# Optimization experiments

Hardware: AMD Instinct MI355X
Metric: run time of the kernel (lower is better)

The kernel has to match this reference:

```python
import jax, jax.numpy as jnp
import numpy as np
from jax import lax

D_MODEL = 512
NUM_HEADS = 8
HEAD_DIM = D_MODEL // NUM_HEADS
KERNEL = 3
B, S = 8, 1024


def _conv1d(x, w, b):
    # x: [B, Cin, S], w: [Cout, Cin, K], 'same' padding, dilation 1
    y = lax.conv_general_dilated(x, w, window_strides=(1,), padding='SAME',
                                 dimension_numbers=('NCH', 'OIH', 'NCH'))
    return y + b[None, :, None]


def setup_inputs() -> dict:
    key = jax.random.key(0)
    ks = jax.random.split(key, 12)
    # conv weight init: normal(0, sqrt(2/(k*out_channels))) with out_channels=head_dim per head;
    # stacking H per-head convs gives a single [D, D, K] weight (head-major out channels).
    std_qk = np.sqrt(2.0 / (KERNEL * HEAD_DIM))
    std_v = np.sqrt(2.0 / (1 * HEAD_DIM))
    inp = {
        'query': jax.random.normal(ks[0], (B, S, D_MODEL), jnp.float32),
        'key_t': jax.random.normal(ks[1], (B, S, D_MODEL), jnp.float32),
        'value': jax.random.normal(ks[2], (B, S, D_MODEL), jnp.float32),
        'Wq': jax.random.normal(ks[3], (D_MODEL, D_MODEL, KERNEL), jnp.float32) * std_qk,
        'bq': jnp.full((D_MODEL,), 0.1, jnp.float32),
        'Wk': jax.random.normal(ks[4], (D_MODEL, D_MODEL, KERNEL), jnp.float32) * std_qk,
        'bk': jnp.full((D_MODEL,), 0.1, jnp.float32),
        'Wv': jax.random.normal(ks[5], (D_MODEL, D_MODEL, 1), jnp.float32) * std_v,
        'bv': jnp.full((D_MODEL,), 0.1, jnp.float32),
        'Wo': jax.random.normal(ks[6], (D_MODEL, D_MODEL), jnp.float32) * (1.0 / np.sqrt(D_MODEL)),
        'bo': jnp.zeros((D_MODEL,), jnp.float32),
    }
    return inp


def reference(query, key_t, value, Wq, bq, Wk, bk, Wv, bv, Wo, bo):
    Bb, Ss, D = query.shape
    H, hd = NUM_HEADS, HEAD_DIM
    # [B, D, S]
    q_ = jnp.transpose(query, (0, 2, 1))
    k_ = jnp.transpose(key_t, (0, 2, 1))
    v_ = jnp.transpose(value, (0, 2, 1))
    # per-head TCN projections fused into one conv; out channels head-major
    Q = _conv1d(q_, Wq, bq).reshape(Bb, H, hd, Ss)
    K = _conv1d(k_, Wk, bk).reshape(Bb, H, hd, Ss)
    V = _conv1d(v_, Wv, bv).reshape(Bb, H, hd, Ss)
    # scores scaled by head_dim (NOT sqrt), as in source
    scores = jnp.einsum('bhds,bhdt->bhst', Q, K) / hd
    attn = jax.nn.softmax(scores, axis=-1)          # [B,H,S,S]
    ave_att = attn.mean(axis=1)                      # [B,S,S]
    out = jnp.einsum('bhst,bhdt->bhsd', attn, V)     # [B,H,S,hd]
    out = jnp.transpose(out, (0, 2, 1, 3)).reshape(Bb, Ss, D)
    out = out @ Wo.T + bo                            # torch Linear: x W^T + b
    return out, ave_att
```

## Files before the change

kernel.cpp:

```cpp
#include <hip/hip_runtime.h>
#include <hip/hip_bf16.h>
#include <math.h>

#define BB 8
#define SS 1024
#define DM 512
#define NH 8
#define HD 64

typedef __attribute__((ext_vector_type(8))) short bf16x8;
typedef __attribute__((ext_vector_type(4))) float f32x4;
typedef __hip_bfloat16 bf16;

static __device__ __forceinline__ short f2bs(float f){
  return __builtin_bit_cast(short, __float2bfloat16(f));
}

static __device__ __forceinline__ float wave_max64(float v){
#pragma unroll
  for (int off = 32; off > 0; off >>= 1) v = fmaxf(v, __shfl_xor(v, off, 64));
  return v;
}
static __device__ __forceinline__ float wave_sum64(float v){
#pragma unroll
  for (int off = 32; off > 0; off >>= 1) v += __shfl_xor(v, off, 64);
  return v;
}

__global__ __launch_bounds__(256) void pack_w(
    const float* __restrict__ Wq, const float* __restrict__ Wk,
    const float* __restrict__ Wv, const float* __restrict__ Wo,
    bf16* __restrict__ Wqb, bf16* __restrict__ Wkb,
    bf16* __restrict__ Wvb, bf16* __restrict__ Wob)
{
  const int idx = blockIdx.x * 256 + threadIdx.x;
#pragma unroll
  for (int k = 0; k < 3; k++){
    Wqb[k * 262144 + idx] = __float2bfloat16(Wq[idx * 3 + k]);
    Wkb[k * 262144 + idx] = __float2bfloat16(Wk[idx * 3 + k]);
  }
  Wvb[idx] = __float2bfloat16(Wv[idx]);
  Wob[idx] = __float2bfloat16(Wo[idx]);
}

template<int KS, bool IN_BF16, bool OUT_F32, bool TROUT>
__global__ __launch_bounds__(256) void gemm_k(const void* __restrict__ xin,
    const bf16* __restrict__ Wb, const float* __restrict__ bias, void* __restrict__ outv)
{
  constexpr int ST = 32;
  constexpr int PAD = (KS - 1) / 2;
  constexpr int NR = ST + KS - 1;
  constexpr int LDX = DM + 8;
  constexpr int SMB_A = NR * LDX * 2;
  constexpr int SMB_B = 32 * 257 * 4;
  constexpr int SMB = (SMB_A > SMB_B) ? SMB_A : SMB_B;
  __shared__ char smem[SMB];
  bf16*  xs = (bf16*)smem;
  float* es = (float*)smem;

  const int b   = blockIdx.x / (SS / ST);
  const int s0  = (blockIdx.x % (SS / ST)) * ST;
  const int tid = threadIdx.x;
  const int w = tid >> 6, l = tid & 63;
  const int lr = l & 15, lg = l >> 4;
  const int o0 = w * 128;

  if (IN_BF16){
    const bf16* x = (const bf16*)xin;
    for (int idx = tid * 4; idx < NR * DM; idx += 1024){
      int r = idx >> 9, c = idx & 511;
      int srow = s0 - PAD + r;
      ushort4 v; v.x = v.y = v.z = v.w = 0;
      if (srow >= 0 && srow < SS)
        v = *reinterpret_cast<const ushort4*>(&x[((size_t)b * SS + srow) * DM + c]);
      *reinterpret_cast<ushort4*>(&xs[r * LDX + c]) = v;
    }
  } else {
    const float* x = (const float*)xin;
    for (int idx = tid * 4; idx < NR * DM; idx += 1024){
      int r = idx >> 9, c = idx & 511;
      int srow = s0 - PAD + r;
      float4 v = make_float4(0.f, 0.f, 0.f, 0.f);
      if (srow >= 0 && srow < SS)
        v = *reinterpret_cast<const float4*>(&x[((size_t)b * SS + srow) * DM + c]);
      ushort4 u;
      u.x = (unsigned short)f2bs(v.x); u.y = (unsigned short)f2bs(v.y);
      u.z = (unsigned short)f2bs(v.z); u.w = (unsigned short)f2bs(v.w);
      *reinterpret_cast<ushort4*>(&xs[r * LDX + c]) = u;
    }
  }

  float bs[8];
#pragma unroll
  for (int of = 0; of < 8; of++) bs[of] = bias[o0 + of * 16 + lr];

  __syncthreads();

  f32x4 acc[2][8];
#pragma unroll
  for (int sf = 0; sf < 2; sf++)
#pragma unroll
    for (int of = 0; of < 8; of++) acc[sf][of] = (f32x4){0.f, 0.f, 0.f, 0.f};

#pragma unroll
  for (int k = 0; k < KS; k++){
    const bf16* wbk = Wb + (size_t)k * DM * DM + (size_t)o0 * DM;
    for (int ic = 0; ic < 16; ic++){
      const int i0 = ic * 32 + lg * 8;
      bf16x8 a0 = *reinterpret_cast<const bf16x8*>(&xs[(lr +      k) * LDX + i0]);
      bf16x8 a1 = *reinterpret_cast<const bf16x8*>(&xs[(lr + 16 + k) * LDX + i0]);
#pragma unroll
      for (int of = 0; of < 8; of++){
        bf16x8 bw = *reinterpret_cast<const bf16x8*>(&wbk[(size_t)(of * 16 + lr) * DM + i0]);
        acc[0][of] = __builtin_amdgcn_mfma_f32_16x16x32_bf16(a0, bw, acc[0][of], 0, 0, 0);
        acc[1][of] = __builtin_amdgcn_mfma_f32_16x16x32_bf16(a1, bw, acc[1][of], 0, 0, 0);
      }
    }
  }

  for (int h2 = 0; h2 < 2; h2++){
    __syncthreads();
    if ((w >> 1) == h2){
      const int ob = (w & 1) * 128;
#pragma unroll
      for (int sf = 0; sf < 2; sf++)
#pragma unroll
        for (int of = 0; of < 8; of++)
#pragma unroll
          for (int r = 0; r < 4; r++)
            es[(sf * 16 + lg * 4 + r) * 257 + ob + of * 16 + lr] = acc[sf][of][r] + bs[of];
    }
    __syncthreads();
    if (!TROUT){
      for (int it = 0; it < 8; it++){
        int t = tid + it * 256;
        int s = t >> 6, c4 = (t & 63) * 4;
        const float* ep = &es[s * 257 + c4];
        if (OUT_F32){
          float* out = (float*)outv;
          float4 v = make_float4(ep[0], ep[1], ep[2], ep[3]);
          *reinterpret_cast<float4*>(&out[((size_t)b * SS + s0 + s) * DM + h2 * 256 + c4]) = v;
        } else {
          bf16* out = (bf16*)outv;
          ushort4 u;
          u.x = (unsigned short)f2bs(ep[0]); u.y = (unsigned short)f2bs(ep[1]);
          u.z = (unsigned short)f2bs(ep[2]); u.w = (unsigned short)f2bs(ep[3]);
          *reinterpret_cast<ushort4*>(&out[((size_t)b * SS + s0 + s) * DM + h2 * 256 + c4]) = u;
        }
      }
    } else {
      bf16* out = (bf16*)outv;
      for (int pass = 0; pass < 8; pass++){
        int oc = pass * 32 + (tid >> 3);
        int s4 = (tid & 7) * 4;
        ushort4 u;
        u.x = (unsigned short)f2bs(es[(s4 + 0) * 257 + oc]);
        u.y = (unsigned short)f2bs(es[(s4 + 1) * 257 + oc]);
        u.z = (unsigned short)f2bs(es[(s4 + 2) * 257 + oc]);
        u.w = (unsigned short)f2bs(es[(s4 + 3) * 257 + oc]);
        int o = h2 * 256 + oc;
        *reinterpret_cast<ushort4*>(&out[((size_t)b * DM + o) * SS + s0 + s4]) = u;
      }
    }
  }
}

#define LDS_SC 1028
__global__ __launch_bounds__(256) void attn2(const bf16* __restrict__ Q,
    const bf16* __restrict__ K, const bf16* __restrict__ Vt,
    bf16* __restrict__ Tw, float* __restrict__ ave)
{
  extern __shared__ float smem[];
  float* scoresL = smem;
  float* aveL    = smem + 16 * LDS_SC;

  const int b   = blockIdx.x >> 6;
  const int s0  = (blockIdx.x & 63) * 16;
  const int tid = threadIdx.x;
  const int w = tid >> 6, l = tid & 63;
  const int lr = l & 15, lg = l >> 4;

  for (int idx = tid; idx < 16 * LDS_SC; idx += 256) aveL[idx] = 0.f;

  const size_t xbase = (size_t)b * SS * DM;
  const size_t vbase = (size_t)b * DM * SS;

  for (int h = 0; h < NH; h++){
    const int hoff = h * HD;
    bf16x8 qa[2];
#pragma unroll
    for (int kk = 0; kk < 2; kk++)
      qa[kk] = *reinterpret_cast<const bf16x8*>(
          &Q[xbase + (size_t)(s0 + lr) * DM + hoff + kk * 32 + lg * 8]);

    for (int tf = 0; tf < 16; tf++){
      const int t0 = w * 256 + tf * 16;
      f32x4 c = (f32x4){0.f, 0.f, 0.f, 0.f};
#pragma unroll
      for (int kk = 0; kk < 2; kk++){
        bf16x8 kb = *reinterpret_cast<const bf16x8*>(
            &K[xbase + (size_t)(t0 + lr) * DM + hoff + kk * 32 + lg * 8]);
        c = __builtin_amdgcn_mfma_f32_16x16x32_bf16(qa[kk], kb, c, 0, 0, 0);
      }
#pragma unroll
      for (int r = 0; r < 4; r++)
        scoresL[(lg * 4 + r) * LDS_SC + t0 + lr] = c[r] * (1.f / 64.f);
    }
    __syncthreads();

    for (int rr = 0; rr < 4; rr++){
      const int q = w * 4 + rr;
      float sv[16];
      float m = -1e30f;
#pragma unroll
      for (int j = 0; j < 16; j++){
        sv[j] = scoresL[q * LDS_SC + l + 64 * j];
        m = fmaxf(m, sv[j]);
      }
      m = wave_max64(m);
      float sum = 0.f;
#pragma unroll
      for (int j = 0; j < 16; j++){ sv[j] = __expf(sv[j] - m); sum += sv[j]; }
      sum = wave_sum64(sum);
      const float inv = 1.f / sum;
#pragma unroll
      for (int j = 0; j < 16; j++){
        const float p = sv[j] * inv;
        scoresL[q * LDS_SC + l + 64 * j] = p;
        aveL[q * LDS_SC + l + 64 * j] += p;
      }
    }
    __syncthreads();

    f32x4 pacc[4];
#pragma unroll
    for (int df = 0; df < 4; df++) pacc[df] = (f32x4){0.f, 0.f, 0.f, 0.f};
    for (int ks8 = 0; ks8 < 8; ks8++){
      const int t0 = w * 256 + ks8 * 32;
      const float* pr = &scoresL[(size_t)lr * LDS_SC + t0 + lg * 8];
      float4 p0 = *reinterpret_cast<const float4*>(pr);
      float4 p1 = *reinterpret_cast<const float4*>(pr + 4);
      bf16x8 pa;
      pa[0] = f2bs(p0.x); pa[1] = f2bs(p0.y); pa[2] = f2bs(p0.z); pa[3] = f2bs(p0.w);
      pa[4] = f2bs(p1.x); pa[5] = f2bs(p1.y); pa[6] = f2bs(p1.z); pa[7] = f2bs(p1.w);
#pragma unroll
      for (int df = 0; df < 4; df++){
        bf16x8 vb = *reinterpret_cast<const bf16x8*>(
            &Vt[vbase + (size_t)(hoff + df * 16 + lr) * SS + t0 + lg * 8]);
        pacc[df] = __builtin_amdgcn_mfma_f32_16x16x32_bf16(pa, vb, pacc[df], 0, 0, 0);
      }
    }
    __syncthreads();

#pragma unroll
    for (int df = 0; df < 4; df++)
#pragma unroll
      for (int r = 0; r < 4; r++)
        scoresL[w * 1040 + (lg * 4 + r) * 65 + df * 16 + lr] = pacc[df][r];
    __syncthreads();
    for (int idx = tid; idx < 1024; idx += 256){
      const int q = idx >> 6, d = idx & 63;
      float s = scoresL[q * 65 + d] + scoresL[1040 + q * 65 + d]
              + scoresL[2080 + q * 65 + d] + scoresL[3120 + q * 65 + d];
      Tw[xbase + (size_t)(s0 + q) * DM + hoff + d] = __float2bfloat16(s);
    }
    __syncthreads();
  }

  for (int idx = tid; idx < 16 * SS; idx += 256){
    const int q = idx >> 10, t = idx & 1023;
    ave[((size_t)b * SS + s0 + q) * SS + t] = aveL[q * LDS_SC + t] * 0.125f;
  }
}

extern "C" void kernel_launch(void* const* d_in, const int* in_sizes, int n_in,
                              void* d_out, int out_size, void* d_ws, size_t ws_size,
                              hipStream_t stream)
{
  const float* query = (const float*)d_in[0];
  const float* key_t = (const float*)d_in[1];
  const float* value = (const float*)d_in[2];
  const float* Wq = (const float*)d_in[3];
  const float* bq = (const float*)d_in[4];
  const float* Wk = (const float*)d_in[5];
  const float* bk = (const float*)d_in[6];
  const float* Wv = (const float*)d_in[7];
  const float* bv = (const float*)d_in[8];
  const float* Wo = (const float*)d_in[9];
  const float* bo = (const float*)d_in[10];

  float* out = (float*)d_out;
  float* ave = out + (size_t)BB * SS * DM;

  char* wsb = (char*)d_ws;
  bf16* Qw  = (bf16*)(wsb);
  bf16* Kw  = (bf16*)(wsb + 8388608);
  bf16* Vt  = (bf16*)(wsb + 16777216);
  bf16* Tw  = (bf16*)(wsb + 25165824);
  bf16* Wqb = (bf16*)(wsb + 33554432);
  bf16* Wkb = (bf16*)(wsb + 35127296);
  bf16* Wvb = (bf16*)(wsb + 36700160);
  bf16* Wob = (bf16*)(wsb + 37224448);

  hipLaunchKernelGGL(pack_w, dim3(1024), dim3(256), 0, stream,
                     Wq, Wk, Wv, Wo, Wqb, Wkb, Wvb, Wob);

  const int g = BB * (SS / 32);
  hipLaunchKernelGGL((gemm_k<3, false, false, false>), dim3(g), dim3(256), 0, stream,
                     (const void*)query, Wqb, bq, (void*)Qw);
  hipLaunchKernelGGL((gemm_k<3, false, false, false>), dim3(g), dim3(256), 0, stream,
                     (const void*)key_t, Wkb, bk, (void*)Kw);
  hipLaunchKernelGGL((gemm_k<1, false, false, true>), dim3(g), dim3(256), 0, stream,
                     (const void*)value, Wvb, bv, (void*)Vt);

  const size_t asmem = (size_t)2 * 16 * LDS_SC * sizeof(float);
  hipFuncSetAttribute((const void*)attn2,
                      hipFuncAttributeMaxDynamicSharedMemorySize, (int)asmem);
  hipLaunchKernelGGL(attn2, dim3(BB * 64), dim3(256), asmem, stream,
                     Qw, Kw, Vt, Tw, ave);

  hipLaunchKernelGGL((gemm_k<1, true, true, false>), dim3(g), dim3(256), 0, stream,
                     (const void*)Tw, Wob, bo, (void*)out);
}
```

Before: 664.5 us.

## Parallelize attention across heads with bf16 prob buffer and separate head-mean reduction

Attention now launches one block per (batch, head, 16-query tile) instead of looping over all heads inside a block. Scores stay in registers for the softmax, and the bf16 probabilities are staged in swizzled LDS and also written to a global buffer. A separate reduce kernel sums that buffer over heads to form the averaged attention map. The projection GEMMs are re-tiled to 16-row tiles, split output halves across blocks, and use an XOR-swizzled LDS layout. This gives far more parallelism, but it adds heavy global traffic for the probability buffer and rounds the averaged map through bf16 probabilities.

```diff
diff --git a/kernel.cpp b/kernel.cpp
--- a/kernel.cpp
+++ b/kernel.cpp
@@ -1,6 +1,5 @@
 #include <hip/hip_runtime.h>
 #include <hip/hip_bf16.h>
-#include <math.h>
 
 #define BB 8
 #define SS 1024
@@ -12,19 +11,8 @@
 typedef __attribute__((ext_vector_type(4))) float f32x4;
 typedef __hip_bfloat16 bf16;
 
-static __device__ __forceinline__ short f2bs(float f){
-  return __builtin_bit_cast(short, __float2bfloat16(f));
-}
-
-static __device__ __forceinline__ float wave_max64(float v){
-#pragma unroll
-  for (int off = 32; off > 0; off >>= 1) v = fmaxf(v, __shfl_xor(v, off, 64));
-  return v;
-}
-static __device__ __forceinline__ float wave_sum64(float v){
-#pragma unroll
-  for (int off = 32; off > 0; off >>= 1) v += __shfl_xor(v, off, 64);
-  return v;
+static __device__ __forceinline__ unsigned short f2bs(float f){
+  return (unsigned short)__builtin_bit_cast(short, __float2bfloat16(f));
 }
 
 __global__ __launch_bounds__(256) void pack_w(
@@ -44,233 +32,247 @@
 }
 
 template<int KS, bool IN_BF16, bool OUT_F32, bool TROUT>
-__global__ __launch_bounds__(256) void gemm_k(const void* __restrict__ xin,
+__global__ __launch_bounds__(256) void gemm2(const void* __restrict__ xin,
     const bf16* __restrict__ Wb, const float* __restrict__ bias, void* __restrict__ outv)
 {
-  constexpr int ST = 32;
+  constexpr int ST = 16;
   constexpr int PAD = (KS - 1) / 2;
   constexpr int NR = ST + KS - 1;
-  constexpr int LDX = DM + 8;
-  constexpr int SMB_A = NR * LDX * 2;
-  constexpr int SMB_B = 32 * 257 * 4;
+  constexpr int SMB_A = NR * 1024;
+  constexpr int SMB_B = 16 * 260 * 4;
   constexpr int SMB = (SMB_A > SMB_B) ? SMB_A : SMB_B;
   __shared__ char smem[SMB];
-  bf16*  xs = (bf16*)smem;
+  char*  xs = smem;
   float* es = (float*)smem;
 
-  const int b   = blockIdx.x / (SS / ST);
-  const int s0  = (blockIdx.x % (SS / ST)) * ST;
+  const int oh = blockIdx.x & 1;
+  const int st = (blockIdx.x >> 1) & 63;
+  const int b  = blockIdx.x >> 7;
+  const int s0 = st * ST;
   const int tid = threadIdx.x;
   const int w = tid >> 6, l = tid & 63;
   const int lr = l & 15, lg = l >> 4;
-  const int o0 = w * 128;
-
-  if (IN_BF16){
-    const bf16* x = (const bf16*)xin;
-    for (int idx = tid * 4; idx < NR * DM; idx += 1024){
-      int r = idx >> 9, c = idx & 511;
-      int srow = s0 - PAD + r;
-      ushort4 v; v.x = v.y = v.z = v.w = 0;
-      if (srow >= 0 && srow < SS)
-        v = *reinterpret_cast<const ushort4*>(&x[((size_t)b * SS + srow) * DM + c]);
-      *reinterpret_cast<ushort4*>(&xs[r * LDX + c]) = v;
+  const int o0 = oh * 256 + w * 64;
+
+  for (int idx = tid * 4; idx < NR * DM; idx += 1024){
+    const int r = idx >> 9, c = idx & 511;
+    const int srow = s0 - PAD + r;
+    const int byte = r * 1024 + ((c * 2) ^ ((r & 7) << 4));
+    if (IN_BF16){
+      ushort4 v = {0, 0, 0, 0};
+      if (0 <= srow && srow < SS)
+        v = *reinterpret_cast<const ushort4*>((const bf16*)xin + ((size_t)b * SS + srow) * DM + c);
+      *reinterpret_cast<ushort4*>(xs + byte) = v;
+    } else {
+      float4 v = make_float4(0.f, 0.f, 0.f, 0.f);
+      if (0 <= srow && srow < SS)
+        v = *reinterpret_cast<const float4*>((const float*)xin + ((size_t)b * SS + srow) * DM + c);
+      ushort4 u; u.x = f2bs(v.x); u.y = f2bs(v.y); u.z = f2bs(v.z); u.w = f2bs(v.w);
+      *reinterpret_cast<ushort4*>(xs + byte) = u;
+    }
+  }
+
+  float bs[4];
+#pragma unroll
+  for (int of = 0; of < 4; of++) bs[of] = bias[o0 + of * 16 + lr];
+
+  __syncthreads();
+
+  f32x4 acc[4];
+#pragma unroll
+  for (int of = 0; of < 4; of++) acc[of] = (f32x4){0.f, 0.f, 0.f, 0.f};
+
+#pragma unroll
+  for (int k = 0; k < KS; k++){
+    const bf16* wbk = Wb + (size_t)k * DM * DM;
+    const int row = lr + k;
+    const int rswz = (row & 7) << 4;
+    for (int ic = 0; ic < 16; ic++){
+      bf16x8 a = *reinterpret_cast<const bf16x8*>(
+          xs + row * 1024 + (((ic * 32 + lg * 8) * 2) ^ rswz));
+#pragma unroll
+      for (int of = 0; of < 4; of++){
+        bf16x8 bw = *reinterpret_cast<const bf16x8*>(
+            wbk + (size_t)(o0 + of * 16 + lr) * DM + ic * 32 + lg * 8);
+        acc[of] = __builtin_amdgcn_mfma_f32_16x16x32_bf16(a, bw, acc[of], 0, 0, 0);
+      }
+    }
+  }
+
+  __syncthreads();
+#pragma unroll
+  for (int of = 0; of < 4; of++)
+#pragma unroll
+    for (int r = 0; r < 4; r++)
+      es[(lg * 4 + r) * 260 + w * 64 + of * 16 + lr] = acc[of][r] + bs[of];
+  __syncthreads();
+
+  if (!TROUT){
+#pragma unroll
+    for (int it = 0; it < 4; it++){
+      const int t = tid + it * 256;
+      const int s = t >> 6, c4 = (t & 63) * 4;
+      const float* ep = &es[s * 260 + c4];
+      if (OUT_F32){
+        float4 v = make_float4(ep[0], ep[1], ep[2], ep[3]);
+        *reinterpret_cast<float4*>((float*)outv + ((size_t)b * SS + s0 + s) * DM + oh * 256 + c4) = v;
+      } else {
+        ushort4 u; u.x = f2bs(ep[0]); u.y = f2bs(ep[1]); u.z = f2bs(ep[2]); u.w = f2bs(ep[3]);
+        *reinterpret_cast<ushort4*>((bf16*)outv + ((size_t)b * SS + s0 + s) * DM + oh * 256 + c4) = u;
+      }
     }
   } else {
-    const float* x = (const float*)xin;
-    for (int idx = tid * 4; idx < NR * DM; idx += 1024){
-      int r = idx >> 9, c = idx & 511;
-      int srow = s0 - PAD + r;
-      float4 v = make_float4(0.f, 0.f, 0.f, 0.f);
-      if (srow >= 0 && srow < SS)
-        v = *reinterpret_cast<const float4*>(&x[((size_t)b * SS + srow) * DM + c]);
-      ushort4 u;
-      u.x = (unsigned short)f2bs(v.x); u.y = (unsigned short)f2bs(v.y);
-      u.z = (unsigned short)f2bs(v.z); u.w = (unsigned short)f2bs(v.w);
-      *reinterpret_cast<ushort4*>(&xs[r * LDX + c]) = u;
-    }
-  }
-
-  float bs[8];
-#pragma unroll
-  for (int of = 0; of < 8; of++) bs[of] = bias[o0 + of * 16 + lr];
-
-  __syncthreads();
-
-  f32x4 acc[2][8];
-#pragma unroll
-  for (int sf = 0; sf < 2; sf++)
-#pragma unroll
-    for (int of = 0; of < 8; of++) acc[sf][of] = (f32x4){0.f, 0.f, 0.f, 0.f};
-
-#pragma unroll
-  for (int k = 0; k < KS; k++){
-    const bf16* wbk = Wb + (size_t)k * DM * DM + (size_t)o0 * DM;
-    for (int ic = 0; ic < 16; ic++){
-      const int i0 = ic * 32 + lg * 8;
-      bf16x8 a0 = *reinterpret_cast<const bf16x8*>(&xs[(lr +      k) * LDX + i0]);
-      bf16x8 a1 = *reinterpret_cast<const bf16x8*>(&xs[(lr + 16 + k) * LDX + i0]);
-#pragma unroll
-      for (int of = 0; of < 8; of++){
-        bf16x8 bw = *reinterpret_cast<const bf16x8*>(&wbk[(size_t)(of * 16 + lr) * DM + i0]);
-        acc[0][of] = __builtin_amdgcn_mfma_f32_16x16x32_bf16(a0, bw, acc[0][of], 0, 0, 0);
-        acc[1][of] = __builtin_amdgcn_mfma_f32_16x16x32_bf16(a1, bw, acc[1][of], 0, 0, 0);
-      }
-    }
-  }
-
-  for (int h2 = 0; h2 < 2; h2++){
-    __syncthreads();
-    if ((w >> 1) == h2){
-      const int ob = (w & 1) * 128;
-#pragma unroll
-      for (int sf = 0; sf < 2; sf++)
-#pragma unroll
-        for (int of = 0; of < 8; of++)
-#pragma unroll
-          for (int r = 0; r < 4; r++)
-            es[(sf * 16 + lg * 4 + r) * 257 + ob + of * 16 + lr] = acc[sf][of][r] + bs[of];
-    }
-    __syncthreads();
-    if (!TROUT){
-      for (int it = 0; it < 8; it++){
-        int t = tid + it * 256;
-        int s = t >> 6, c4 = (t & 63) * 4;
-        const float* ep = &es[s * 257 + c4];
-        if (OUT_F32){
-          float* out = (float*)outv;
-          float4 v = make_float4(ep[0], ep[1], ep[2], ep[3]);
-          *reinterpret_cast<float4*>(&out[((size_t)b * SS + s0 + s) * DM + h2 * 256 + c4]) = v;
-        } else {
-          bf16* out = (bf16*)outv;
-          ushort4 u;
-          u.x = (unsigned short)f2bs(ep[0]); u.y = (unsigned short)f2bs(ep[1]);
-          u.z = (unsigned short)f2bs(ep[2]); u.w = (unsigned short)f2bs(ep[3]);
-          *reinterpret_cast<ushort4*>(&out[((size_t)b * SS + s0 + s) * DM + h2 * 256 + c4]) = u;
-        }
-      }
-    } else {
-      bf16* out = (bf16*)outv;
-      for (int pass = 0; pass < 8; pass++){
-        int oc = pass * 32 + (tid >> 3);
-        int s4 = (tid & 7) * 4;
-        ushort4 u;
-        u.x = (unsigned short)f2bs(es[(s4 + 0) * 257 + oc]);
-        u.y = (unsigned short)f2bs(es[(s4 + 1) * 257 + oc]);
-        u.z = (unsigned short)f2bs(es[(s4 + 2) * 257 + oc]);
-        u.w = (unsigned short)f2bs(es[(s4 + 3) * 257 + oc]);
-        int o = h2 * 256 + oc;
-        *reinterpret_cast<ushort4*>(&out[((size_t)b * DM + o) * SS + s0 + s4]) = u;
-      }
-    }
-  }
-}
-
-#define LDS_SC 1028
-__global__ __launch_bounds__(256) void attn2(const bf16* __restrict__ Q,
+    const int o = oh * 256 + tid;
+    uint us[8];
+#pragma unroll
+    for (int j = 0; j < 8; j++){
+      const float lo = es[(2 * j) * 260 + tid];
+      const float hi = es[(2 * j + 1) * 260 + tid];
+      us[j] = (uint)f2bs(lo) | ((uint)f2bs(hi) << 16);
+    }
+    uint4* dst = reinterpret_cast<uint4*>((bf16*)outv + ((size_t)b * DM + o) * SS + s0);
+    dst[0] = make_uint4(us[0], us[1], us[2], us[3]);
+    dst[1] = make_uint4(us[4], us[5], us[6], us[7]);
+  }
+}
+
+template<int HG>
+__global__ __launch_bounds__(256) void attn3(const bf16* __restrict__ Q,
     const bf16* __restrict__ K, const bf16* __restrict__ Vt,
-    bf16* __restrict__ Tw, float* __restrict__ ave)
-{
-  extern __shared__ float smem[];
-  float* scoresL = smem;
-  float* aveL    = smem + 16 * LDS_SC;
-
-  const int b   = blockIdx.x >> 6;
-  const int s0  = (blockIdx.x & 63) * 16;
-  const int tid = threadIdx.x;
+    bf16* __restrict__ Tw, bf16* __restrict__ Pbuf, int h0)
+{
+  __shared__ char smem[33280];
+  char*  plds = smem;
+  float* red  = (float*)smem;
+  float* mxL  = (float*)(smem + 32768);
+  float* smL  = (float*)(smem + 33024);
+
+  const int qt   = blockIdx.x & 63;
+  const int rest = blockIdx.x >> 6;
+  const int hl   = rest & (HG - 1);
+  const int b    = rest / HG;
+  const int h    = h0 + hl;
+  const int s0   = qt * 16;
+  const int tid  = threadIdx.x;
   const int w = tid >> 6, l = tid & 63;
   const int lr = l & 15, lg = l >> 4;
-
-  for (int idx = tid; idx < 16 * LDS_SC; idx += 256) aveL[idx] = 0.f;
-
-  const size_t xbase = (size_t)b * SS * DM;
+  const int hoff = h * HD;
+  const size_t xb = (size_t)b * SS * DM;
+
+  bf16x8 qb0 = *reinterpret_cast<const bf16x8*>(&Q[xb + (size_t)(s0 + lr) * DM + hoff + lg * 8]);
+  bf16x8 qb1 = *reinterpret_cast<const bf16x8*>(&Q[xb + (size_t)(s0 + lr) * DM + hoff + 32 + lg * 8]);
+
+  f32x4 sc[16];
+#pragma unroll
+  for (int tf = 0; tf < 16; tf++){
+    const int t0 = w * 256 + tf * 16;
+    bf16x8 ka0 = *reinterpret_cast<const bf16x8*>(&K[xb + (size_t)(t0 + lr) * DM + hoff + lg * 8]);
+    bf16x8 ka1 = *reinterpret_cast<const bf16x8*>(&K[xb + (size_t)(t0 + lr) * DM + hoff + 32 + lg * 8]);
+    f32x4 c = (f32x4){0.f, 0.f, 0.f, 0.f};
+    c = __builtin_amdgcn_mfma_f32_16x16x32_bf16(ka0, qb0, c, 0, 0, 0);
+    c = __builtin_amdgcn_mfma_f32_16x16x32_bf16(ka1, qb1, c, 0, 0, 0);
+#pragma unroll
+    for (int r = 0; r < 4; r++) sc[tf][r] = c[r] * (1.f / 64.f);
+  }
+
+  float m = -1e30f;
+#pragma unroll
+  for (int tf = 0; tf < 16; tf++)
+#pragma unroll
+    for (int r = 0; r < 4; r++) m = fmaxf(m, sc[tf][r]);
+  m = fmaxf(m, __shfl_xor(m, 16, 64));
+  m = fmaxf(m, __shfl_xor(m, 32, 64));
+  if (l < 16) mxL[w * 16 + l] = m;
+  __syncthreads();
+  m = fmaxf(fmaxf(mxL[lr], mxL[16 + lr]), fmaxf(mxL[32 + lr], mxL[48 + lr]));
+
+  float sum = 0.f;
+#pragma unroll
+  for (int tf = 0; tf < 16; tf++)
+#pragma unroll
+    for (int r = 0; r < 4; r++){ sc[tf][r] = __expf(sc[tf][r] - m); sum += sc[tf][r]; }
+  sum += __shfl_xor(sum, 16, 64);
+  sum += __shfl_xor(sum, 32, 64);
+  if (l < 16) smL[w * 16 + l] = sum;
+  __syncthreads();
+  const float inv = 1.f / (smL[lr] + smL[16 + lr] + smL[32 + lr] + smL[48 + lr]);
+
+  const size_t pb = (((size_t)b * HG + hl) * SS + (s0 + lr)) * SS;
+  const int swz = (lr & 7) << 4;
+#pragma unroll
+  for (int tf = 0; tf < 16; tf++){
+    const int t = w * 256 + tf * 16 + lg * 4;
+    const uint u0 = (uint)f2bs(sc[tf][0] * inv) | ((uint)f2bs(sc[tf][1] * inv) << 16);
+    const uint u1 = (uint)f2bs(sc[tf][2] * inv) | ((uint)f2bs(sc[tf][3] * inv) << 16);
+    *reinterpret_cast<uint2*>(plds + lr * 2048 + ((2 * t) ^ swz)) = make_uint2(u0, u1);
+    *reinterpret_cast<uint2*>((char*)Pbuf + 2 * (pb + t)) = make_uint2(u0, u1);
+  }
+
   const size_t vbase = (size_t)b * DM * SS;
-
-  for (int h = 0; h < NH; h++){
-    const int hoff = h * HD;
-    bf16x8 qa[2];
-#pragma unroll
-    for (int kk = 0; kk < 2; kk++)
-      qa[kk] = *reinterpret_cast<const bf16x8*>(
-          &Q[xbase + (size_t)(s0 + lr) * DM + hoff + kk * 32 + lg * 8]);
-
-    for (int tf = 0; tf < 16; tf++){
-      const int t0 = w * 256 + tf * 16;
-      f32x4 c = (f32x4){0.f, 0.f, 0.f, 0.f};
-#pragma unroll
-      for (int kk = 0; kk < 2; kk++){
-        bf16x8 kb = *reinterpret_cast<const bf16x8*>(
-            &K[xbase + (size_t)(t0 + lr) * DM + hoff + kk * 32 + lg * 8]);
-        c = __builtin_amdgcn_mfma_f32_16x16x32_bf16(qa[kk], kb, c, 0, 0, 0);
-      }
-#pragma unroll
-      for (int r = 0; r < 4; r++)
-        scoresL[(lg * 4 + r) * LDS_SC + t0 + lr] = c[r] * (1.f / 64.f);
-    }
-    __syncthreads();
-
-    for (int rr = 0; rr < 4; rr++){
-      const int q = w * 4 + rr;
-      float sv[16];
-      float m = -1e30f;
-#pragma unroll
-      for (int j = 0; j < 16; j++){
-        sv[j] = scoresL[q * LDS_SC + l + 64 * j];
-        m = fmaxf(m, sv[j]);
-      }
-      m = wave_max64(m);
-      float sum = 0.f;
-#pragma unroll
-      for (int j = 0; j < 16; j++){ sv[j] = __expf(sv[j] - m); sum += sv[j]; }
-      sum = wave_sum64(sum);
-      const float inv = 1.f / sum;
-#pragma unroll
-      for (int j = 0; j < 16; j++){
-        const float p = sv[j] * inv;
-        scoresL[q * LDS_SC + l + 64 * j] = p;
-        aveL[q * LDS_SC + l + 64 * j] += p;
-      }
-    }
-    __syncthreads();
-
-    f32x4 pacc[4];
-#pragma unroll
-    for (int df = 0; df < 4; df++) pacc[df] = (f32x4){0.f, 0.f, 0.f, 0.f};
-    for (int ks8 = 0; ks8 < 8; ks8++){
-      const int t0 = w * 256 + ks8 * 32;
-      const float* pr = &scoresL[(size_t)lr * LDS_SC + t0 + lg * 8];
-      float4 p0 = *reinterpret_cast<const float4*>(pr);
-      float4 p1 = *reinterpret_cast<const float4*>(pr + 4);
-      bf16x8 pa;
-      pa[0] = f2bs(p0.x); pa[1] = f2bs(p0.y); pa[2] = f2bs(p0.z); pa[3] = f2bs(p0.w);
-      pa[4] = f2bs(p1.x); pa[5] = f2bs(p1.y); pa[6] = f2bs(p1.z); pa[7] = f2bs(p1.w);
-#pragma unroll
-      for (int df = 0; df < 4; df++){
-        bf16x8 vb = *reinterpret_cast<const bf16x8*>(
-            &Vt[vbase + (size_t)(hoff + df * 16 + lr) * SS + t0 + lg * 8]);
-        pacc[df] = __builtin_amdgcn_mfma_f32_16x16x32_bf16(pa, vb, pacc[df], 0, 0, 0);
-      }
-    }
-    __syncthreads();
-
-#pragma unroll
-    for (int df = 0; df < 4; df++)
-#pragma unroll
-      for (int r = 0; r < 4; r++)
-        scoresL[w * 1040 + (lg * 4 + r) * 65 + df * 16 + lr] = pacc[df][r];
-    __syncthreads();
-    for (int idx = tid; idx < 1024; idx += 256){
-      const int q = idx >> 6, d = idx & 63;
-      float s = scoresL[q * 65 + d] + scoresL[1040 + q * 65 + d]
-              + scoresL[2080 + q * 65 + d] + scoresL[3120 + q * 65 + d];
-      Tw[xbase + (size_t)(s0 + q) * DM + hoff + d] = __float2bfloat16(s);
-    }
-    __syncthreads();
-  }
-
-  for (int idx = tid; idx < 16 * SS; idx += 256){
-    const int q = idx >> 10, t = idx & 1023;
-    ave[((size_t)b * SS + s0 + q) * SS + t] = aveL[q * LDS_SC + t] * 0.125f;
-  }
+  f32x4 pacc[4];
+#pragma unroll
+  for (int df = 0; df < 4; df++) pacc[df] = (f32x4){0.f, 0.f, 0.f, 0.f};
+#pragma unroll
+  for (int ks = 0; ks < 8; ks++){
+    bf16x8 pa = *reinterpret_cast<const bf16x8*>(
+        plds + lr * 2048 + ((w * 512 + ks * 64 + lg * 16) ^ swz));
+#pragma unroll
+    for (int df = 0; df < 4; df++){
+      bf16x8 vv = *reinterpret_cast<const bf16x8*>(
+          &Vt[vbase + (size_t)(hoff + df * 16 + lr) * SS + w * 256 + ks * 32 + lg * 8]);
+      pacc[df] = __builtin_amdgcn_mfma_f32_16x16x32_bf16(pa, vv, pacc[df], 0, 0, 0);
+    }
+  }
+  __syncthreads();
+#pragma unroll
+  for (int df = 0; df < 4; df++)
+#pragma unroll
+    for (int r = 0; r < 4; r++)
+      red[w * 1040 + (lg * 4 + r) * 65 + df * 16 + lr] = pacc[df][r];
+  __syncthreads();
+  {
+    const int q = tid >> 4, d4 = (tid & 15) * 4;
+    float o[4];
+#pragma unroll
+    for (int j = 0; j < 4; j++)
+      o[j] = red[q * 65 + d4 + j] + red[1040 + q * 65 + d4 + j]
+           + red[2080 + q * 65 + d4 + j] + red[3120 + q * 65 + d4 + j];
+    ushort4 u; u.x = f2bs(o[0]); u.y = f2bs(o[1]); u.z = f2bs(o[2]); u.w = f2bs(o[3]);
+    *reinterpret_cast<ushort4*>(&Tw[xb + (size_t)(s0 + q) * DM + hoff + d4]) = u;
+  }
+}
+
+__global__ __launch_bounds__(256) void reduce_p(const bf16* __restrict__ P,
+    float* __restrict__ ave, int nh, int first)
+{
+  const int idx = blockIdx.x * 256 + threadIdx.x;
+  const int b = idx >> 17;
+  const int rem = idx & 131071;
+  const int q = rem >> 7;
+  const int c8 = (rem & 127) * 8;
+  float a[8] = {0.f, 0.f, 0.f, 0.f, 0.f, 0.f, 0.f, 0.f};
+  for (int hl = 0; hl < nh; hl++){
+    const uint4 v = *reinterpret_cast<const uint4*>(
+        &P[(((size_t)b * nh + hl) * SS + q) * SS + c8]);
+    const uint uu[4] = {v.x, v.y, v.z, v.w};
+#pragma unroll
+    for (int j = 0; j < 4; j++){
+      a[2 * j]     += __uint_as_float(uu[j] << 16);
+      a[2 * j + 1] += __uint_as_float(uu[j] & 0xFFFF0000u);
+    }
+  }
+  float* op = &ave[((size_t)b * SS + q) * SS + c8];
+  float r[8];
+#pragma unroll
+  for (int j = 0; j < 8; j++) r[j] = a[j] * 0.125f;
+  if (!first){
+    const float4 e0 = *reinterpret_cast<const float4*>(op);
+    const float4 e1 = *reinterpret_cast<const float4*>(op + 4);
+    r[0] += e0.x; r[1] += e0.y; r[2] += e0.z; r[3] += e0.w;
+    r[4] += e1.x; r[5] += e1.y; r[6] += e1.z; r[7] += e1.w;
+  }
+  *reinterpret_cast<float4*>(op)     = make_float4(r[0], r[1], r[2], r[3]);
+  *reinterpret_cast<float4*>(op + 4) = make_float4(r[4], r[5], r[6], r[7]);
 }
 
 extern "C" void kernel_launch(void* const* d_in, const int* in_sizes, int n_in,
@@ -301,24 +303,38 @@
   bf16* Wkb = (bf16*)(wsb + 35127296);
   bf16* Wvb = (bf16*)(wsb + 36700160);
   bf16* Wob = (bf16*)(wsb + 37224448);
+  bf16* Pb  = (bf16*)(wsb + 37748736);
 
   hipLaunchKernelGGL(pack_w, dim3(1024), dim3(256), 0, stream,
                      Wq, Wk, Wv, Wo, Wqb, Wkb, Wvb, Wob);
 
-  const int g = BB * (SS / 32);
-  hipLaunchKernelGGL((gemm_k<3, false, false, false>), dim3(g), dim3(256), 0, stream,
+  hipLaunchKernelGGL((gemm2<3, false, false, false>), dim3(1024), dim3(256), 0, stream,
                      (const void*)query, Wqb, bq, (void*)Qw);
-  hipLaunchKernelGGL((gemm_k<3, false, false, false>), dim3(g), dim3(256), 0, stream,
+  hipLaunchKernelGGL((gemm2<3, false, false, false>), dim3(1024), dim3(256), 0, stream,
                      (const void*)key_t, Wkb, bk, (void*)Kw);
-  hipLaunchKernelGGL((gemm_k<1, false, false, true>), dim3(g), dim3(256), 0, stream,
+  hipLaunchKernelGGL((gemm2<1, false, false, true>), dim3(1024), dim3(256), 0, stream,
                      (const void*)value, Wvb, bv, (void*)Vt);
 
-  const size_t asmem = (size_t)2 * 16 * LDS_SC * sizeof(float);
-  hipFuncSetAttribute((const void*)attn2,
-                      hipFuncAttributeMaxDynamicSharedMemorySize, (int)asmem);
-  hipLaunchKernelGGL(attn2, dim3(BB * 64), dim3(256), asmem, stream,
-                     Qw, Kw, Vt, Tw, ave);
-
-  hipLaunchKernelGGL((gemm_k<1, true, true, false>), dim3(g), dim3(256), 0, stream,
+  const size_t base = 37748736ull;
+  int G;
+  if      (ws_size >= base + 134217728ull) G = 1;
+  else if (ws_size >= base +  67108864ull) G = 2;
+  else if (ws_size >= base +  33554432ull) G = 4;
+  else                                     G = 8;
+  const int HG = NH / G;
+
+  for (int g = 0; g < G; g++){
+    const dim3 grid(BB * HG * 64);
+    const int h0 = g * HG;
+    switch (HG){
+      case 8: hipLaunchKernelGGL((attn3<8>), grid, dim3(256), 0, stream, Qw, Kw, Vt, Tw, Pb, h0); break;
+      case 4: hipLaunchKernelGGL((attn3<4>), grid, dim3(256), 0, stream, Qw, Kw, Vt, Tw, Pb, h0); break;
+      case 2: hipLaunchKernelGGL((attn3<2>), grid, dim3(256), 0, stream, Qw, Kw, Vt, Tw, Pb, h0); break;
+      default: hipLaunchKernelGGL((attn3<1>), grid, dim3(256), 0, stream, Qw, Kw, Vt, Tw, Pb, h0); break;
+    }
+    hipLaunchKernelGGL(reduce_p, dim3(4096), dim3(256), 0, stream, Pb, ave, HG, g == 0 ? 1 : 0);
+  }
+
+  hipLaunchKernelGGL((gemm2<1, true, true, false>), dim3(1024), dim3(256), 0, stream,
                      (const void*)Tw, Wob, bo, (void*)out);
 }
```

New measurement: 534.3 us. 19.6% less time.
